# Kernel optimization log

Hardware: AMD Instinct MI355X
Metric: run time of the kernel (lower is better)

The kernel has to match this reference:

```python
import jax, jax.numpy as jnp
import numpy as np

B, T, C, HS = 4, 2048, 1024, 64

def setup_inputs() -> dict:
    key = jax.random.key(0)
    k1, k2, k3, k4 = jax.random.split(key, 4)
    x = jax.random.normal(k1, (B, T, C), dtype=jnp.float32)
    # torch Linear default init scale ~ 1/sqrt(fan_in); scale weights similarly
    s = C ** -0.5
    Wq = jax.random.normal(k2, (C, HS), dtype=jnp.float32) * s
    Wk = jax.random.normal(k3, (C, HS), dtype=jnp.float32) * s
    Wv = jax.random.normal(k4, (C, HS), dtype=jnp.float32) * s
    return {"x": x, "Wq": Wq, "Wk": Wk, "Wv": Wv}

def reference(x, Wq, Wk, Wv):
    B_, T_, C_ = x.shape
    q = x @ Wq          # [B,T,HS]
    k = x @ Wk          # [B,T,HS]
    v = x @ Wv          # [B,T,HS]
    scale = C_ ** -0.5  # note: module scales by input dim C, not head_size
    w = jnp.einsum('bqh,bkh->bqk', q, k) * scale  # [B,T,T]
    causal = jnp.tril(jnp.ones((T_, T_), dtype=bool))
    w = jnp.where(causal, w, -jnp.inf)
    a = jax.nn.softmax(w, axis=-1)  # dropout is identity (eval / drop_rate=0)
    return jnp.einsum('bqk,bkh->bqh', a, v)
```

## Files before the change

### kernel.cpp

```cpp
#include <hip/hip_runtime.h>
#include <math.h>

#define B_  4
#define T_  2048
#define C_  1024
#define HS_ 64
#define M_  (B_*T_)
#define NCAT 192
#define SCALE_ 0.03125f
#define XPAD 1032

typedef unsigned short ushort_t;
typedef short bf16x8 __attribute__((ext_vector_type(8)));
typedef float f32x4 __attribute__((ext_vector_type(4)));

static __device__ __forceinline__ unsigned short f2bf(float f) {
    union { float f; unsigned int u; } c; c.f = f;
    unsigned int u = c.u;
    return (unsigned short)((u + 0x7FFFu + ((u >> 16) & 1u)) >> 16);
}
static __device__ __forceinline__ unsigned short f2bf_fast(float f) {
    union { float f; unsigned int u; } c; c.f = f;
    return (unsigned short)((c.u + 0x8000u) >> 16);
}

__global__ void wconv_kernel(const float* __restrict__ Wq, const float* __restrict__ Wk,
                             const float* __restrict__ Wv, ushort_t* __restrict__ wtp) {
    int l = threadIdx.x & 63;
    int g = blockIdx.x * 4 + (threadIdx.x >> 6);
    int c  = g / 12;
    int nt = g % 12;
    const float* W = (nt < 4) ? Wq : (nt < 8) ? Wk : Wv;
    int nn = (nt & 3) * 16 + (l & 15);
    int k0 = c * 32 + (l >> 4) * 8;
    union { bf16x8 v; ushort_t u[8]; } pk;
    #pragma unroll
    for (int e = 0; e < 8; e++)
        pk.u[e] = f2bf(W[(size_t)(k0 + e) * HS_ + nn]);
    *(bf16x8*)(wtp + ((size_t)g * 64 + l) * 8) = pk.v;
}

__global__ __launch_bounds__(512, 4) void proj_kernel(const float* __restrict__ x,
    const ushort_t* __restrict__ wtp,
    ushort_t* __restrict__ qws, ushort_t* __restrict__ kws, ushort_t* __restrict__ vt) {
    __shared__ __align__(16) unsigned char pool[49152];

    int tid  = threadIdx.x;
    int wid  = tid >> 6;
    int lane = tid & 63;
    int qd   = lane >> 4;
    int lq   = lane & 15;
    int r0   = blockIdx.x * 16;

    ushort_t* xs = (ushort_t*)pool;
    {
        float4 xv[8];
        #pragma unroll
        for (int j = 0; j < 8; j++) {
            int flat4 = j * 512 + tid;
            int row   = flat4 >> 8;
            int c4    = flat4 & 255;
            xv[j] = *(const float4*)(x + (size_t)(r0 + row) * C_ + c4 * 4);
        }
        #pragma unroll
        for (int j = 0; j < 8; j++) {
            int flat4 = j * 512 + tid;
            int row   = flat4 >> 8;
            int c4    = flat4 & 255;
            uint2 p;
            p.x = (unsigned)f2bf(xv[j].x) | ((unsigned)f2bf(xv[j].y) << 16);
            p.y = (unsigned)f2bf(xv[j].z) | ((unsigned)f2bf(xv[j].w) << 16);
            *(uint2*)(xs + row * XPAD + c4 * 4) = p;
        }
    }
    __syncthreads();

    f32x4 acc[12];
    #pragma unroll
    for (int i = 0; i < 12; i++) acc[i] = (f32x4){0.f,0.f,0.f,0.f};

    const ushort_t* xrow = xs + lq * XPAD + wid * 128 + qd * 8;
    #pragma unroll
    for (int i = 0; i < 4; i++) {
        bf16x8 af = *(const bf16x8*)(xrow + i * 32);
        #pragma unroll
        for (int nt = 0; nt < 12; nt++) {
            bf16x8 bv = *(const bf16x8*)(wtp +
                (((size_t)(wid * 4 + i) * 12 + nt) * 64 + lane) * 8);
            acc[nt] = __builtin_amdgcn_mfma_f32_16x16x32_bf16(af, bv, acc[nt], 0, 0, 0);
        }
    }

    __syncthreads();
    f32x4 (*red)[12 * 64] = (f32x4 (*)[12 * 64])pool;
    if (wid >= 4) {
        #pragma unroll
        for (int nt = 0; nt < 12; nt++) red[wid - 4][nt * 64 + lane] = acc[nt];
    }
    __syncthreads();
    if (wid < 4) {
        #pragma unroll
        for (int nt = 0; nt < 12; nt++) acc[nt] += red[wid][nt * 64 + lane];
    }
    __syncthreads();
    if (wid == 2 || wid == 3) {
        #pragma unroll
        for (int nt = 0; nt < 12; nt++) red[wid][nt * 64 + lane] = acc[nt];
    }
    __syncthreads();
    if (wid < 2) {
        #pragma unroll
        for (int nt = 0; nt < 12; nt++) acc[nt] += red[wid + 2][nt * 64 + lane];
    }
    __syncthreads();
    if (wid == 1) {
        #pragma unroll
        for (int nt = 0; nt < 12; nt++) red[0][nt * 64 + lane] = acc[nt];
    }
    __syncthreads();
    if (wid == 0) {
        #pragma unroll
        for (int nt = 0; nt < 12; nt++) {
            acc[nt] += red[0][nt * 64 + lane];
            int outn = nt >> 2;
            int col  = (nt & 3) * 16 + lq;
            #pragma unroll
            for (int r = 0; r < 4; r++) {
                int row = r0 + qd * 4 + r;
                float v = acc[nt][r];
                if (outn == 0) v *= SCALE_;
                ushort_t val = f2bf(v);
                if (outn == 0)      qws[(size_t)row * HS_ + col] = val;
                else if (outn == 1) kws[(size_t)row * HS_ + col] = val;
                else {
                    int b = row >> 11, t = row & 2047;
                    vt[((size_t)b * 64 + col) * T_ + t] = val;
                }
            }
        }
    }
}

__global__ __launch_bounds__(512, 2) void flash_kernel(const ushort_t* __restrict__ qws,
    const ushort_t* __restrict__ kws, const ushort_t* __restrict__ vt,
    float* __restrict__ out) {
    __shared__ __align__(16) unsigned char pool[18432];

    int tid  = threadIdx.x;
    int wid  = tid >> 6;
    int lane = tid & 63;
    int qd   = lane >> 4;
    int lq   = lane & 15;

    int bid   = (int)blockIdx.x;
    int batch = bid & 3;
    int p     = bid >> 2;

    ushort_t* pw = (ushort_t*)pool + wid * 1152 + lq * 72;
    const ushort_t* kp    = kws + (size_t)batch * T_ * HS_;
    const ushort_t* vbase = vt  + (size_t)batch * 64 * T_;
    f32x4* red  = (f32x4*)pool;
    float* lred = (float*)(pool + 16384);

    #pragma unroll 1
    for (int ph = 0; ph < 2; ph++) {
        int tile = ph ? (127 - p) : p;
        int q0   = tile * 16;
        int qrow = q0 + lq;
        int grow = batch * T_ + qrow;
        int nU   = (tile + 4) >> 2;

        bf16x8 qf[2];
        #pragma unroll
        for (int st = 0; st < 2; st++)
            qf[st] = *(const bf16x8*)(qws + (size_t)grow * HS_ + st * 32 + qd * 8);

        float lsum = 0.f;
        f32x4 O[4];
        #pragma unroll
        for (int nt = 0; nt < 4; nt++) O[nt] = (f32x4){0.f,0.f,0.f,0.f};

        #pragma unroll 1
        for (int u = wid; u < nU; u += 8) {
            int kb = u * 64;

            bf16x8 kf[8], vf[8];
            #pragma unroll
            for (int sub = 0; sub < 4; sub++)
                #pragma unroll
                for (int st = 0; st < 2; st++)
                    kf[sub * 2 + st] = *(const bf16x8*)(kp + (size_t)(kb + sub * 16 + lq) * HS_ + st * 32 + qd * 8);
            #pragma unroll
            for (int nt = 0; nt < 4; nt++)
                #pragma unroll
                for (int kk = 0; kk < 2; kk++)
                    vf[nt * 2 + kk] = *(const bf16x8*)(vbase + ((size_t)nt * 16 + lq) * T_ + kb + kk * 32 + qd * 8);
            __builtin_amdgcn_sched_barrier(0);

            f32x4 S[4];
            #pragma unroll
            for (int sub = 0; sub < 4; sub++) {
                f32x4 s = (f32x4){0.f,0.f,0.f,0.f};
                #pragma unroll
                for (int st = 0; st < 2; st++)
                    s = __builtin_amdgcn_mfma_f32_16x16x32_bf16(kf[sub * 2 + st], qf[st], s, 0, 0, 0);
                S[sub] = s;
            }

            if (kb + 64 > q0) {
                #pragma unroll
                for (int sub = 0; sub < 4; sub++)
                    #pragma unroll
                    for (int r = 0; r < 4; r++) {
                        int key = kb + sub * 16 + qd * 4 + r;
                        float pv = (key <= qrow) ? __expf(S[sub][r]) : 0.f;
                        S[sub][r] = pv;
                        lsum += pv;
                    }
            } else {
                #pragma unroll
                for (int sub = 0; sub < 4; sub++)
                    #pragma unroll
                    for (int r = 0; r < 4; r++) {
                        float pv = __expf(S[sub][r]);
                        S[sub][r] = pv;
                        lsum += pv;
                    }
            }

            #pragma unroll
            for (int sub = 0; sub < 4; sub++) {
                uint2 d;
                d.x = (unsigned)f2bf_fast(S[sub][0]) | ((unsigned)f2bf_fast(S[sub][1]) << 16);
                d.y = (unsigned)f2bf_fast(S[sub][2]) | ((unsigned)f2bf_fast(S[sub][3]) << 16);
                *(uint2*)(pw + sub * 16 + qd * 4) = d;
            }
            bf16x8 pf0 = *(const bf16x8*)(pw + qd * 8);
            bf16x8 pf1 = *(const bf16x8*)(pw + 32 + qd * 8);

            #pragma unroll
            for (int nt = 0; nt < 4; nt++) {
                O[nt] = __builtin_amdgcn_mfma_f32_16x16x32_bf16(vf[nt * 2 + 0], pf0, O[nt], 0, 0, 0);
                O[nt] = __builtin_amdgcn_mfma_f32_16x16x32_bf16(vf[nt * 2 + 1], pf1, O[nt], 0, 0, 0);
            }
        }

        __syncthreads();
        if (wid >= 4) {
            f32x4* rs = red + (size_t)(wid - 4) * 256;
            #pragma unroll
            for (int nt = 0; nt < 4; nt++) rs[nt * 64 + lane] = O[nt];
            lred[(wid - 4) * 64 + lane] = lsum;
        }
        __syncthreads();
        if (wid < 4) {
            f32x4* rs = red + (size_t)wid * 256;
            #pragma unroll
            for (int nt = 0; nt < 4; nt++) O[nt] += rs[nt * 64 + lane];
            lsum += lred[wid * 64 + lane];
        }
        __syncthreads();
        if (wid == 2 || wid == 3) {
            f32x4* rs = red + (size_t)(wid - 2) * 256;
            #pragma unroll
            for (int nt = 0; nt < 4; nt++) rs[nt * 64 + lane] = O[nt];
            lred[(wid - 2) * 64 + lane] = lsum;
        }
        __syncthreads();
        if (wid < 2) {
            f32x4* rs = red + (size_t)wid * 256;
            #pragma unroll
            for (int nt = 0; nt < 4; nt++) O[nt] += rs[nt * 64 + lane];
            lsum += lred[wid * 64 + lane];
        }
        __syncthreads();
        if (wid == 1) {
            #pragma unroll
            for (int nt = 0; nt < 4; nt++) red[nt * 64 + lane] = O[nt];
            lred[lane] = lsum;
        }
        __syncthreads();
        if (wid == 0) {
            #pragma unroll
            for (int nt = 0; nt < 4; nt++) O[nt] += red[nt * 64 + lane];
            lsum += lred[lane];
            lsum += __shfl_xor(lsum, 16, 64);
            lsum += __shfl_xor(lsum, 32, 64);
            float li = 1.f / lsum;
            #pragma unroll
            for (int nt = 0; nt < 4; nt++) {
                f32x4 o = O[nt] * li;
                *(f32x4*)(out + (size_t)grow * HS_ + nt * 16 + qd * 4) = o;
            }
        }
        __syncthreads();
    }
}

extern "C" void kernel_launch(void* const* d_in, const int* in_sizes, int n_in,
                              void* d_out, int out_size, void* d_ws, size_t ws_size,
                              hipStream_t stream) {
    const float* x  = (const float*)d_in[0];
    const float* Wq = (const float*)d_in[1];
    const float* Wk = (const float*)d_in[2];
    const float* Wv = (const float*)d_in[3];
    float* out = (float*)d_out;

    ushort_t* wtp = (ushort_t*)d_ws;
    ushort_t* qws = wtp + (size_t)384 * 64 * 8;
    ushort_t* kws = qws + (size_t)M_ * HS_;
    ushort_t* vt  = kws + (size_t)M_ * HS_;

    wconv_kernel<<<96, 256, 0, stream>>>(Wq, Wk, Wv, wtp);
    proj_kernel<<<512, 512, 0, stream>>>(x, wtp, qws, kws, vt);
    flash_kernel<<<256, 512, 0, stream>>>(qws, kws, vt, out);
}
```

Measured before the change: 107.3 us.

## Fuse weight conversion, projection and attention into one persistent kernel with flags

Merges the three launches into a single 512-block kernel. The first 48 blocks convert the weights to bf16 while every block spins on a global counter. Each block then projects its own 16 rows and sets a ready flag, and finally runs attention for one query tile after waiting on the flags of the key/value rows it needs. This removes two kernel launches and the gaps between them. In exchange it adds a memset, spin-wait synchronization that relies on all 512 blocks being co-resident, and it drops the previous balanced pairing of short and long causal tiles per block.

```diff
diff --git a/kernel.cpp b/kernel.cpp
--- a/kernel.cpp
+++ b/kernel.cpp
@@ -24,25 +24,11 @@
     return (unsigned short)((c.u + 0x8000u) >> 16);
 }
 
-__global__ void wconv_kernel(const float* __restrict__ Wq, const float* __restrict__ Wk,
-                             const float* __restrict__ Wv, ushort_t* __restrict__ wtp) {
-    int l = threadIdx.x & 63;
-    int g = blockIdx.x * 4 + (threadIdx.x >> 6);
-    int c  = g / 12;
-    int nt = g % 12;
-    const float* W = (nt < 4) ? Wq : (nt < 8) ? Wk : Wv;
-    int nn = (nt & 3) * 16 + (l & 15);
-    int k0 = c * 32 + (l >> 4) * 8;
-    union { bf16x8 v; ushort_t u[8]; } pk;
-    #pragma unroll
-    for (int e = 0; e < 8; e++)
-        pk.u[e] = f2bf(W[(size_t)(k0 + e) * HS_ + nn]);
-    *(bf16x8*)(wtp + ((size_t)g * 64 + l) * 8) = pk.v;
-}
-
-__global__ __launch_bounds__(512, 4) void proj_kernel(const float* __restrict__ x,
-    const ushort_t* __restrict__ wtp,
-    ushort_t* __restrict__ qws, ushort_t* __restrict__ kws, ushort_t* __restrict__ vt) {
+__global__ __launch_bounds__(512, 2) void fused_kernel(const float* __restrict__ x,
+    const float* __restrict__ Wq, const float* __restrict__ Wk,
+    const float* __restrict__ Wv, ushort_t* __restrict__ wtp,
+    ushort_t* __restrict__ qws, ushort_t* __restrict__ kws, ushort_t* __restrict__ vt,
+    int* __restrict__ flags, float* __restrict__ out) {
     __shared__ __align__(16) unsigned char pool[49152];
 
     int tid  = threadIdx.x;
@@ -50,111 +36,157 @@
     int lane = tid & 63;
     int qd   = lane >> 4;
     int lq   = lane & 15;
-    int r0   = blockIdx.x * 16;
-
-    ushort_t* xs = (ushort_t*)pool;
+    int b    = (int)blockIdx.x;
+
+    int* wcount = flags;
+    int* rflags = flags + 16;
+
+    if (b < 48) {
+        int g  = b * 8 + wid;
+        int c  = g / 12;
+        int nt = g % 12;
+        const float* W = (nt < 4) ? Wq : (nt < 8) ? Wk : Wv;
+        int nn = (nt & 3) * 16 + (lane & 15);
+        int k0 = c * 32 + (lane >> 4) * 8;
+        union { bf16x8 v; ushort_t u[8]; } pk;
+        #pragma unroll
+        for (int e = 0; e < 8; e++)
+            pk.u[e] = f2bf(W[(size_t)(k0 + e) * HS_ + nn]);
+        *(bf16x8*)(wtp + ((size_t)g * 64 + lane) * 8) = pk.v;
+        __threadfence();
+        __syncthreads();
+        if (tid == 0) atomicAdd(wcount, 1);
+    }
+
+    if (tid == 0) {
+        while (atomicAdd(wcount, 0) < 48) __builtin_amdgcn_s_sleep(2);
+    }
+    __syncthreads();
+    __builtin_amdgcn_fence(__ATOMIC_ACQUIRE, "agent");
+
     {
-        float4 xv[8];
-        #pragma unroll
-        for (int j = 0; j < 8; j++) {
-            int flat4 = j * 512 + tid;
-            int row   = flat4 >> 8;
-            int c4    = flat4 & 255;
-            xv[j] = *(const float4*)(x + (size_t)(r0 + row) * C_ + c4 * 4);
-        }
-        #pragma unroll
-        for (int j = 0; j < 8; j++) {
-            int flat4 = j * 512 + tid;
-            int row   = flat4 >> 8;
-            int c4    = flat4 & 255;
-            uint2 p;
-            p.x = (unsigned)f2bf(xv[j].x) | ((unsigned)f2bf(xv[j].y) << 16);
-            p.y = (unsigned)f2bf(xv[j].z) | ((unsigned)f2bf(xv[j].w) << 16);
-            *(uint2*)(xs + row * XPAD + c4 * 4) = p;
-        }
-    }
-    __syncthreads();
-
-    f32x4 acc[12];
-    #pragma unroll
-    for (int i = 0; i < 12; i++) acc[i] = (f32x4){0.f,0.f,0.f,0.f};
-
-    const ushort_t* xrow = xs + lq * XPAD + wid * 128 + qd * 8;
-    #pragma unroll
-    for (int i = 0; i < 4; i++) {
-        bf16x8 af = *(const bf16x8*)(xrow + i * 32);
-        #pragma unroll
-        for (int nt = 0; nt < 12; nt++) {
-            bf16x8 bv = *(const bf16x8*)(wtp +
-                (((size_t)(wid * 4 + i) * 12 + nt) * 64 + lane) * 8);
-            acc[nt] = __builtin_amdgcn_mfma_f32_16x16x32_bf16(af, bv, acc[nt], 0, 0, 0);
-        }
-    }
-
-    __syncthreads();
-    f32x4 (*red)[12 * 64] = (f32x4 (*)[12 * 64])pool;
-    if (wid >= 4) {
-        #pragma unroll
-        for (int nt = 0; nt < 12; nt++) red[wid - 4][nt * 64 + lane] = acc[nt];
-    }
-    __syncthreads();
-    if (wid < 4) {
-        #pragma unroll
-        for (int nt = 0; nt < 12; nt++) acc[nt] += red[wid][nt * 64 + lane];
-    }
-    __syncthreads();
-    if (wid == 2 || wid == 3) {
-        #pragma unroll
-        for (int nt = 0; nt < 12; nt++) red[wid][nt * 64 + lane] = acc[nt];
-    }
-    __syncthreads();
-    if (wid < 2) {
-        #pragma unroll
-        for (int nt = 0; nt < 12; nt++) acc[nt] += red[wid + 2][nt * 64 + lane];
-    }
-    __syncthreads();
-    if (wid == 1) {
-        #pragma unroll
-        for (int nt = 0; nt < 12; nt++) red[0][nt * 64 + lane] = acc[nt];
-    }
-    __syncthreads();
-    if (wid == 0) {
-        #pragma unroll
-        for (int nt = 0; nt < 12; nt++) {
-            acc[nt] += red[0][nt * 64 + lane];
-            int outn = nt >> 2;
-            int col  = (nt & 3) * 16 + lq;
-            #pragma unroll
-            for (int r = 0; r < 4; r++) {
-                int row = r0 + qd * 4 + r;
-                float v = acc[nt][r];
-                if (outn == 0) v *= SCALE_;
-                ushort_t val = f2bf(v);
-                if (outn == 0)      qws[(size_t)row * HS_ + col] = val;
-                else if (outn == 1) kws[(size_t)row * HS_ + col] = val;
-                else {
-                    int b = row >> 11, t = row & 2047;
-                    vt[((size_t)b * 64 + col) * T_ + t] = val;
+        int r0 = b * 16;
+        ushort_t* xs = (ushort_t*)pool;
+        {
+            float4 xv[8];
+            #pragma unroll
+            for (int j = 0; j < 8; j++) {
+                int flat4 = j * 512 + tid;
+                int row   = flat4 >> 8;
+                int c4    = flat4 & 255;
+                xv[j] = *(const float4*)(x + (size_t)(r0 + row) * C_ + c4 * 4);
+            }
+            #pragma unroll
+            for (int j = 0; j < 8; j++) {
+                int flat4 = j * 512 + tid;
+                int row   = flat4 >> 8;
+                int c4    = flat4 & 255;
+                uint2 p;
+                p.x = (unsigned)f2bf(xv[j].x) | ((unsigned)f2bf(xv[j].y) << 16);
+                p.y = (unsigned)f2bf(xv[j].z) | ((unsigned)f2bf(xv[j].w) << 16);
+                *(uint2*)(xs + row * XPAD + c4 * 4) = p;
+            }
+        }
+        __syncthreads();
+
+        f32x4 acc[12];
+        #pragma unroll
+        for (int i = 0; i < 12; i++) acc[i] = (f32x4){0.f,0.f,0.f,0.f};
+
+        const ushort_t* xrow = xs + lq * XPAD + wid * 128 + qd * 8;
+        #pragma unroll
+        for (int i = 0; i < 4; i++) {
+            bf16x8 af = *(const bf16x8*)(xrow + i * 32);
+            #pragma unroll
+            for (int nt = 0; nt < 12; nt++) {
+                bf16x8 bv = *(const bf16x8*)(wtp +
+                    (((size_t)(wid * 4 + i) * 12 + nt) * 64 + lane) * 8);
+                acc[nt] = __builtin_amdgcn_mfma_f32_16x16x32_bf16(af, bv, acc[nt], 0, 0, 0);
+            }
+        }
+
+        __syncthreads();
+        f32x4 (*red)[12 * 64] = (f32x4 (*)[12 * 64])pool;
+        if (wid >= 4) {
+            #pragma unroll
+            for (int nt = 0; nt < 12; nt++) red[wid - 4][nt * 64 + lane] = acc[nt];
+        }
+        __syncthreads();
+        if (wid < 4) {
+            #pragma unroll
+            for (int nt = 0; nt < 12; nt++) acc[nt] += red[wid][nt * 64 + lane];
+        }
+        __syncthreads();
+        if (wid == 2 || wid == 3) {
+            #pragma unroll
+            for (int nt = 0; nt < 12; nt++) red[wid][nt * 64 + lane] = acc[nt];
+        }
+        __syncthreads();
+        if (wid < 2) {
+            #pragma unroll
+            for (int nt = 0; nt < 12; nt++) acc[nt] += red[wid + 2][nt * 64 + lane];
+        }
+        __syncthreads();
+        if (wid == 1) {
+            #pragma unroll
+            for (int nt = 0; nt < 12; nt++) red[0][nt * 64 + lane] = acc[nt];
+        }
+        __syncthreads();
+        if (wid == 0) {
+            #pragma unroll
+            for (int nt = 0; nt < 12; nt++) {
+                acc[nt] += red[0][nt * 64 + lane];
+                int outn = nt >> 2;
+                int col  = (nt & 3) * 16 + lq;
+                #pragma unroll
+                for (int r = 0; r < 4; r++) {
+                    int row = r0 + qd * 4 + r;
+                    float v = acc[nt][r];
+                    if (outn == 0) v *= SCALE_;
+                    ushort_t val = f2bf(v);
+                    if (outn == 0)      qws[(size_t)row * HS_ + col] = val;
+                    else if (outn == 1) kws[(size_t)row * HS_ + col] = val;
+                    else {
+                        int bb2 = row >> 11, t2 = row & 2047;
+                        vt[((size_t)bb2 * 64 + t2 * 0 + col) * T_ + t2] = val;
+                    }
                 }
             }
-        }
-    }
-}
-
-__global__ __launch_bounds__(512, 2) void flash_kernel(const ushort_t* __restrict__ qws,
-    const ushort_t* __restrict__ kws, const ushort_t* __restrict__ vt,
-    float* __restrict__ out) {
-    __shared__ __align__(16) unsigned char pool[18432];
-
-    int tid  = threadIdx.x;
-    int wid  = tid >> 6;
-    int lane = tid & 63;
-    int qd   = lane >> 4;
-    int lq   = lane & 15;
-
-    int bid   = (int)blockIdx.x;
-    int batch = bid & 3;
-    int p     = bid >> 2;
+            __threadfence();
+        }
+        __syncthreads();
+        if (tid == 0) atomicExch(&rflags[b], 1);
+    }
+
+    int batch = b >> 7;
+    int t     = b & 127;
+    int q0    = t * 16;
+    int qrow  = q0 + lq;
+    int grow  = batch * T_ + qrow;
+    int nU    = (t + 4) >> 2;
+    int lastl = 4 * nU - 1; if (lastl > 127) lastl = 127;
+
+    if (tid == 0) {
+        int base = batch * 128;
+        int i = base;
+        int end = base + lastl;
+        while (i <= end) {
+            if (atomicAdd(&rflags[i], 0) != 0) i++;
+            else __builtin_amdgcn_s_sleep(2);
+        }
+    }
+    __syncthreads();
+    __builtin_amdgcn_fence(__ATOMIC_ACQUIRE, "agent");
+
+    bf16x8 qf[2];
+    #pragma unroll
+    for (int st = 0; st < 2; st++)
+        qf[st] = *(const bf16x8*)(qws + (size_t)grow * HS_ + st * 32 + qd * 8);
+
+    float lsum = 0.f;
+    f32x4 O[4];
+    #pragma unroll
+    for (int nt = 0; nt < 4; nt++) O[nt] = (f32x4){0.f,0.f,0.f,0.f};
 
     ushort_t* pw = (ushort_t*)pool + wid * 1152 + lq * 72;
     const ushort_t* kp    = kws + (size_t)batch * T_ * HS_;
@@ -163,137 +195,117 @@
     float* lred = (float*)(pool + 16384);
 
     #pragma unroll 1
-    for (int ph = 0; ph < 2; ph++) {
-        int tile = ph ? (127 - p) : p;
-        int q0   = tile * 16;
-        int qrow = q0 + lq;
-        int grow = batch * T_ + qrow;
-        int nU   = (tile + 4) >> 2;
-
-        bf16x8 qf[2];
-        #pragma unroll
-        for (int st = 0; st < 2; st++)
-            qf[st] = *(const bf16x8*)(qws + (size_t)grow * HS_ + st * 32 + qd * 8);
-
-        float lsum = 0.f;
-        f32x4 O[4];
-        #pragma unroll
-        for (int nt = 0; nt < 4; nt++) O[nt] = (f32x4){0.f,0.f,0.f,0.f};
-
-        #pragma unroll 1
-        for (int u = wid; u < nU; u += 8) {
-            int kb = u * 64;
-
-            bf16x8 kf[8], vf[8];
+    for (int u = wid; u < nU; u += 8) {
+        int kb = u * 64;
+
+        bf16x8 kf[8], vf[8];
+        #pragma unroll
+        for (int sub = 0; sub < 4; sub++)
+            #pragma unroll
+            for (int st = 0; st < 2; st++)
+                kf[sub * 2 + st] = *(const bf16x8*)(kp + (size_t)(kb + sub * 16 + lq) * HS_ + st * 32 + qd * 8);
+        #pragma unroll
+        for (int nt = 0; nt < 4; nt++)
+            #pragma unroll
+            for (int kk = 0; kk < 2; kk++)
+                vf[nt * 2 + kk] = *(const bf16x8*)(vbase + ((size_t)nt * 16 + lq) * T_ + kb + kk * 32 + qd * 8);
+        __builtin_amdgcn_sched_barrier(0);
+
+        f32x4 S[4];
+        #pragma unroll
+        for (int sub = 0; sub < 4; sub++) {
+            f32x4 s = (f32x4){0.f,0.f,0.f,0.f};
+            #pragma unroll
+            for (int st = 0; st < 2; st++)
+                s = __builtin_amdgcn_mfma_f32_16x16x32_bf16(kf[sub * 2 + st], qf[st], s, 0, 0, 0);
+            S[sub] = s;
+        }
+
+        if (kb + 64 > q0) {
             #pragma unroll
             for (int sub = 0; sub < 4; sub++)
                 #pragma unroll
-                for (int st = 0; st < 2; st++)
-                    kf[sub * 2 + st] = *(const bf16x8*)(kp + (size_t)(kb + sub * 16 + lq) * HS_ + st * 32 + qd * 8);
-            #pragma unroll
-            for (int nt = 0; nt < 4; nt++)
+                for (int r = 0; r < 4; r++) {
+                    int key = kb + sub * 16 + qd * 4 + r;
+                    float pv = (key <= qrow) ? __expf(S[sub][r]) : 0.f;
+                    S[sub][r] = pv;
+                    lsum += pv;
+                }
+        } else {
+            #pragma unroll
+            for (int sub = 0; sub < 4; sub++)
                 #pragma unroll
-                for (int kk = 0; kk < 2; kk++)
-                    vf[nt * 2 + kk] = *(const bf16x8*)(vbase + ((size_t)nt * 16 + lq) * T_ + kb + kk * 32 + qd * 8);
-            __builtin_amdgcn_sched_barrier(0);
-
-            f32x4 S[4];
-            #pragma unroll
-            for (int sub = 0; sub < 4; sub++) {
-                f32x4 s = (f32x4){0.f,0.f,0.f,0.f};
-                #pragma unroll
-                for (int st = 0; st < 2; st++)
-                    s = __builtin_amdgcn_mfma_f32_16x16x32_bf16(kf[sub * 2 + st], qf[st], s, 0, 0, 0);
-                S[sub] = s;
-            }
-
-            if (kb + 64 > q0) {
-                #pragma unroll
-                for (int sub = 0; sub < 4; sub++)
-                    #pragma unroll
-                    for (int r = 0; r < 4; r++) {
-                        int key = kb + sub * 16 + qd * 4 + r;
-                        float pv = (key <= qrow) ? __expf(S[sub][r]) : 0.f;
-                        S[sub][r] = pv;
-                        lsum += pv;
-                    }
-            } else {
-                #pragma unroll
-                for (int sub = 0; sub < 4; sub++)
-                    #pragma unroll
-                    for (int r = 0; r < 4; r++) {
-                        float pv = __expf(S[sub][r]);
-                        S[sub][r] = pv;
-                        lsum += pv;
-                    }
-            }
-
-            #pragma unroll
-            for (int sub = 0; sub < 4; sub++) {
-                uint2 d;
-                d.x = (unsigned)f2bf_fast(S[sub][0]) | ((unsigned)f2bf_fast(S[sub][1]) << 16);
-                d.y = (unsigned)f2bf_fast(S[sub][2]) | ((unsigned)f2bf_fast(S[sub][3]) << 16);
-                *(uint2*)(pw + sub * 16 + qd * 4) = d;
-            }
-            bf16x8 pf0 = *(const bf16x8*)(pw + qd * 8);
-            bf16x8 pf1 = *(const bf16x8*)(pw + 32 + qd * 8);
-
-            #pragma unroll
-            for (int nt = 0; nt < 4; nt++) {
-                O[nt] = __builtin_amdgcn_mfma_f32_16x16x32_bf16(vf[nt * 2 + 0], pf0, O[nt], 0, 0, 0);
-                O[nt] = __builtin_amdgcn_mfma_f32_16x16x32_bf16(vf[nt * 2 + 1], pf1, O[nt], 0, 0, 0);
-            }
-        }
-
-        __syncthreads();
-        if (wid >= 4) {
-            f32x4* rs = red + (size_t)(wid - 4) * 256;
-            #pragma unroll
-            for (int nt = 0; nt < 4; nt++) rs[nt * 64 + lane] = O[nt];
-            lred[(wid - 4) * 64 + lane] = lsum;
-        }
-        __syncthreads();
-        if (wid < 4) {
-            f32x4* rs = red + (size_t)wid * 256;
-            #pragma unroll
-            for (int nt = 0; nt < 4; nt++) O[nt] += rs[nt * 64 + lane];
-            lsum += lred[wid * 64 + lane];
-        }
-        __syncthreads();
-        if (wid == 2 || wid == 3) {
-            f32x4* rs = red + (size_t)(wid - 2) * 256;
-            #pragma unroll
-            for (int nt = 0; nt < 4; nt++) rs[nt * 64 + lane] = O[nt];
-            lred[(wid - 2) * 64 + lane] = lsum;
-        }
-        __syncthreads();
-        if (wid < 2) {
-            f32x4* rs = red + (size_t)wid * 256;
-            #pragma unroll
-            for (int nt = 0; nt < 4; nt++) O[nt] += rs[nt * 64 + lane];
-            lsum += lred[wid * 64 + lane];
-        }
-        __syncthreads();
-        if (wid == 1) {
-            #pragma unroll
-            for (int nt = 0; nt < 4; nt++) red[nt * 64 + lane] = O[nt];
-            lred[lane] = lsum;
-        }
-        __syncthreads();
-        if (wid == 0) {
-            #pragma unroll
-            for (int nt = 0; nt < 4; nt++) O[nt] += red[nt * 64 + lane];
-            lsum += lred[lane];
-            lsum += __shfl_xor(lsum, 16, 64);
-            lsum += __shfl_xor(lsum, 32, 64);
-            float li = 1.f / lsum;
-            #pragma unroll
-            for (int nt = 0; nt < 4; nt++) {
-                f32x4 o = O[nt] * li;
-                *(f32x4*)(out + (size_t)grow * HS_ + nt * 16 + qd * 4) = o;
-            }
-        }
-        __syncthreads();
+                for (int r = 0; r < 4; r++) {
+                    float pv = __expf(S[sub][r]);
+                    S[sub][r] = pv;
+                    lsum += pv;
+                }
+        }
+
+        #pragma unroll
+        for (int sub = 0; sub < 4; sub++) {
+            uint2 d;
+            d.x = (unsigned)f2bf_fast(S[sub][0]) | ((unsigned)f2bf_fast(S[sub][1]) << 16);
+            d.y = (unsigned)f2bf_fast(S[sub][2]) | ((unsigned)f2bf_fast(S[sub][3]) << 16);
+            *(uint2*)(pw + sub * 16 + qd * 4) = d;
+        }
+        bf16x8 pf0 = *(const bf16x8*)(pw + qd * 8);
+        bf16x8 pf1 = *(const bf16x8*)(pw + 32 + qd * 8);
+
+        #pragma unroll
+        for (int nt = 0; nt < 4; nt++) {
+            O[nt] = __builtin_amdgcn_mfma_f32_16x16x32_bf16(vf[nt * 2 + 0], pf0, O[nt], 0, 0, 0);
+            O[nt] = __builtin_amdgcn_mfma_f32_16x16x32_bf16(vf[nt * 2 + 1], pf1, O[nt], 0, 0, 0);
+        }
+    }
+
+    __syncthreads();
+    if (wid >= 4) {
+        f32x4* rs = red + (size_t)(wid - 4) * 256;
+        #pragma unroll
+        for (int nt = 0; nt < 4; nt++) rs[nt * 64 + lane] = O[nt];
+        lred[(wid - 4) * 64 + lane] = lsum;
+    }
+    __syncthreads();
+    if (wid < 4) {
+        f32x4* rs = red + (size_t)wid * 256;
+        #pragma unroll
+        for (int nt = 0; nt < 4; nt++) O[nt] += rs[nt * 64 + lane];
+        lsum += lred[wid * 64 + lane];
+    }
+    __syncthreads();
+    if (wid == 2 || wid == 3) {
+        f32x4* rs = red + (size_t)(wid - 2) * 256;
+        #pragma unroll
+        for (int nt = 0; nt < 4; nt++) rs[nt * 64 + lane] = O[nt];
+        lred[(wid - 2) * 64 + lane] = lsum;
+    }
+    __syncthreads();
+    if (wid < 2) {
+        f32x4* rs = red + (size_t)wid * 256;
+        #pragma unroll
+        for (int nt = 0; nt < 4; nt++) O[nt] += rs[nt * 64 + lane];
+        lsum += lred[wid * 64 + lane];
+    }
+    __syncthreads();
+    if (wid == 1) {
+        #pragma unroll
+        for (int nt = 0; nt < 4; nt++) red[nt * 64 + lane] = O[nt];
+        lred[lane] = lsum;
+    }
+    __syncthreads();
+    if (wid == 0) {
+        #pragma unroll
+        for (int nt = 0; nt < 4; nt++) O[nt] += red[nt * 64 + lane];
+        lsum += lred[lane];
+        lsum += __shfl_xor(lsum, 16, 64);
+        lsum += __shfl_xor(lsum, 32, 64);
+        float li = 1.f / lsum;
+        #pragma unroll
+        for (int nt = 0; nt < 4; nt++) {
+            f32x4 o = O[nt] * li;
+            *(f32x4*)(out + (size_t)grow * HS_ + nt * 16 + qd * 4) = o;
+        }
     }
 }
 
@@ -310,8 +322,10 @@
     ushort_t* qws = wtp + (size_t)384 * 64 * 8;
     ushort_t* kws = qws + (size_t)M_ * HS_;
     ushort_t* vt  = kws + (size_t)M_ * HS_;
-
-    wconv_kernel<<<96, 256, 0, stream>>>(Wq, Wk, Wv, wtp);
-    proj_kernel<<<512, 512, 0, stream>>>(x, wtp, qws, kws, vt);
-    flash_kernel<<<256, 512, 0, stream>>>(qws, kws, vt, out);
+    int* flags    = (int*)(vt + (size_t)M_ * HS_);
+
+    hipMemsetAsync(flags, 0, (16 + 512) * sizeof(int), stream);
+    void* args[] = {(void*)&x, (void*)&Wq, (void*)&Wk, (void*)&Wv, (void*)&wtp,
+                    (void*)&qws, (void*)&kws, (void*)&vt, (void*)&flags, (void*)&out};
+    hipLaunchKernel((const void*)fused_kernel, dim3(512), dim3(512), args, 0, stream);
 }
```

Result: slower. 202.9 us (+89.0%).
